# Kernel tuning notes

Measured on AMD Instinct MI355X. Metric: run time of the kernel, lower is better.

## Reference

```python
import jax, jax.numpy as jnp
import numpy as np

NEG = -1e9
BN_EPS = 1e-3  # keras BatchNormalization default epsilon
LRELU = 0.2    # GAT leaky-relu slope


def _gat(Xt, bias_mat, Wg, a1, a2, bg):
    """Dense multi-head GAT (Velickovic TF impl).
    Xt: [B,N,F], bias_mat: [B,N,N] additive mask (0 / -1e9).
    Wg: [H,F,D], a1/a2/bg: [H,D]. Returns [B,N,H*D]."""
    feats = jnp.einsum('bnf,hfd->bhnd', Xt, Wg)          # [B,H,N,D]
    f1 = jnp.einsum('bhnd,hd->bhn', feats, a1)
    f2 = jnp.einsum('bhnd,hd->bhn', feats, a2)
    logits = f1[:, :, :, None] + f2[:, :, None, :]        # [B,H,N,N]
    logits = jax.nn.leaky_relu(logits, LRELU) + bias_mat[:, None]
    coefs = jax.nn.softmax(logits, axis=-1)
    vals = jnp.einsum('bhnm,bhmd->bhnd', coefs, feats) + bg[None, :, None, :]
    vals = jax.nn.elu(vals)
    B, H, N, D = vals.shape
    return jnp.transpose(vals, (0, 2, 1, 3)).reshape(B, N, H * D)


def setup_inputs() -> dict:
    key = jax.random.key(0)
    ks = jax.random.split(key, 16)
    B, T, N, F = 4, 12, 2048, 64
    H, D = 4, 16           # attn_heads, hid_units
    C = H * D              # out_channels = 64

    X = jax.random.normal(ks[0], (B, T, N, F), dtype=jnp.float32)
    # random sparse adjacency (~avg degree 16) + self loops -> additive mask
    adj = jax.random.uniform(ks[1], (B, N, N)) < (16.0 / N)
    adj = adj | jnp.eye(N, dtype=bool)[None]
    bias_mat = jnp.where(adj, 0.0, NEG).astype(jnp.float32)

    he = lambda k, s: jax.random.normal(k, s, dtype=jnp.float32) * np.sqrt(2.0 / s[-2] if len(s) > 1 else 2.0 / s[-1])
    return {
        'X': X, 'bias_mat': bias_mat,
        'W_z': he(ks[2], (F, C)), 'Z_bias': he(ks[3], (1, C)),
        'W_h': he(ks[4], (F, C)), 'H_bias': he(ks[5], (1, C)),
        'Wg_z': he(ks[6], (H, F, D)), 'a1_z': he(ks[7], (H, D)),
        'a2_z': he(ks[8], (H, D)), 'bg_z': jnp.zeros((H, D), jnp.float32),
        'Wg_h': he(ks[9], (H, F, D)), 'a1_h': he(ks[10], (H, D)),
        'a2_h': he(ks[11], (H, D)), 'bg_h': jnp.zeros((H, D), jnp.float32),
        'bn_gamma': jnp.ones((C,), jnp.float32), 'bn_beta': jnp.zeros((C,), jnp.float32),
        'bn_mean': jnp.zeros((C,), jnp.float32), 'bn_var': jnp.ones((C,), jnp.float32),
    }


def reference(X, bias_mat, W_z, Z_bias, W_h, H_bias,
              Wg_z, a1_z, a2_z, bg_z, Wg_h, a1_h, a2_h, bg_h,
              bn_gamma, bn_beta, bn_mean, bn_var):
    B, T, N, F = X.shape
    C = W_z.shape[1]
    H0 = jnp.zeros((B, N, C), dtype=jnp.float32)

    def step(Hc, Xt):
        Z = _gat(Xt, bias_mat, Wg_z, a1_z, a2_z, bg_z) + Xt @ W_z + Z_bias + Hc
        Z = jax.nn.sigmoid(Z)
        Tt = _gat(Xt, bias_mat, Wg_h, a1_h, a2_h, bg_h) + Hc + Xt @ W_h + H_bias
        Tt = jnp.tanh(Tt)
        Hn = Z * Hc + (1.0 - Z) * Tt
        return Hn, None

    Xs = jnp.transpose(X, (1, 0, 2, 3))  # [T,B,N,F]
    Hf, _ = jax.lax.scan(step, H0, Xs)
    # last_layer=True path: BatchNorm (inference, moving stats) on final H
    out = (Hf - bn_mean) * jax.lax.rsqrt(bn_var + BN_EPS) * bn_gamma + bn_beta
    return out
```

## Files before the change

kernel.cpp:

```cpp
#include <hip/hip_runtime.h>
#include <cstdint>
#include <cstddef>

#define NB 4
#define NT 12
#define NN 2048
#define NF 64
#define NH 4
#define ND 16
#define NC 64
#define MAXD 64
#define NR (NB * NT * NN)

typedef _Float16 f16x8 __attribute__((ext_vector_type(8)));
typedef _Float16 f16x2 __attribute__((ext_vector_type(2)));
typedef float f32x4 __attribute__((ext_vector_type(4)));

#define LR(v) ((v) >= 0.f ? (v) : 0.2f * (v))
#define RCPF(x) __builtin_amdgcn_rcpf(x)

#define MACLO(acc, w, d)                                                      \
  asm("v_fma_mix_f32 %0, %1, %2, %0 op_sel:[0,0,0] op_sel_hi:[0,1,0]"         \
      : "+v"(acc) : "v"(w), "v"(d))
#define MACHI(acc, w, d)                                                      \
  asm("v_fma_mix_f32 %0, %1, %2, %0 op_sel:[0,1,0] op_sel_hi:[0,1,0]"         \
      : "+v"(acc) : "v"(w), "v"(d))

__global__ __launch_bounds__(256) void build_adj_k(const float* __restrict__ bias,
                                                   int* __restrict__ adj,
                                                   int* __restrict__ deg) {
  int gtid = blockIdx.x * 256 + threadIdx.x;
  int wid = gtid >> 6;
  int lane = threadIdx.x & 63;
  if (wid >= NB * NN) return;
  const float* row = bias + (size_t)wid * NN;
  int* arow = adj + (size_t)wid * MAXD;
  int count = 0;
  for (int c0 = 0; c0 < NN; c0 += 64) {
    float v = __builtin_nontemporal_load(row + c0 + lane);
    bool e = (v > -1e8f);
    unsigned long long m = __ballot(e);
    int pre = __popcll(m & ((1ull << lane) - 1ull));
    if (e) {
      int pos = count + pre;
      if (pos < MAXD) arow[pos] = c0 + lane;
    }
    count += __popcll(m);
  }
  if (lane == 0) deg[wid] = count < MAXD ? count : MAXD;
}

__global__ __launch_bounds__(256) void prep_w_k(
    const float* __restrict__ Wgz, const float* __restrict__ Wgh,
    const float* __restrict__ Wz,  const float* __restrict__ Wh,
    const float* __restrict__ a1z, const float* __restrict__ a2z,
    const float* __restrict__ a1h, const float* __restrict__ a2h,
    const float* __restrict__ Zb,  const float* __restrict__ Hb,
    _Float16* __restrict__ W16, float* __restrict__ biasC) {
  int idx = blockIdx.x * 256 + threadIdx.x;
  if (idx < 272 * 64) {
    int c = idx >> 6, k = idx & 63;
    float w;
    if (c < 64)       w = Wgz[((c >> 4) << 10) + (k << 4) + (c & 15)];
    else if (c < 128) { int q = c - 64; w = Wgh[((q >> 4) << 10) + (k << 4) + (q & 15)]; }
    else if (c < 192) w = Wz[(k << 6) + (c - 128)];
    else if (c < 256) w = Wh[(k << 6) + (c - 192)];
    else {
      int j = c - 256, h = j & 3;
      const float* Wg = (j & 4) ? Wgh : Wgz;
      const float* av = (j & 8) ? ((j & 4) ? a2h : a2z) : ((j & 4) ? a1h : a1z);
      float s = 0.f;
#pragma unroll
      for (int d = 0; d < 16; d++)
        s = fmaf(Wg[(h << 10) + (k << 4) + d], av[(h << 4) + d], s);
      w = s;
    }
    W16[idx] = (_Float16)w;
  }
  if (blockIdx.x == 0 && threadIdx.x < 128)
    biasC[threadIdx.x] =
        (threadIdx.x < 64) ? Zb[threadIdx.x] : Hb[threadIdx.x - 64];
}

__global__ __launch_bounds__(256) void mfma_gemm_k(
    const float* __restrict__ X, const _Float16* __restrict__ W16,
    const float* __restrict__ biasC,
    uint32_t* __restrict__ gbufF, uint32_t* __restrict__ gbufS,
    float* __restrict__ fbuf) {
  __shared__ uint32_t tr[4][16 * 68];
  const int tid = threadIdx.x;
  const int wv = tid >> 6, lane = tid & 63;
  const int m = lane & 15, quad = lane >> 4;
  const unsigned rw = blockIdx.x * 64 + wv * 16;
  uint32_t* tw = tr[wv];

  const float* xr = X + (size_t)(rw + m) * 64;
  float4 x0 = *(const float4*)(xr + quad * 8);
  float4 x1 = *(const float4*)(xr + quad * 8 + 4);
  float4 x2 = *(const float4*)(xr + 32 + quad * 8);
  float4 x3 = *(const float4*)(xr + 32 + quad * 8 + 4);
  f16x8 A0 = {(_Float16)x0.x, (_Float16)x0.y, (_Float16)x0.z, (_Float16)x0.w,
              (_Float16)x1.x, (_Float16)x1.y, (_Float16)x1.z, (_Float16)x1.w};
  f16x8 A1 = {(_Float16)x2.x, (_Float16)x2.y, (_Float16)x2.z, (_Float16)x2.w,
              (_Float16)x3.x, (_Float16)x3.y, (_Float16)x3.z, (_Float16)x3.w};

  float bzc[4], bhc[4];
#pragma unroll
  for (int j = 0; j < 4; j++) {
    bzc[j] = biasC[j * 16 + m];
    bhc[j] = biasC[64 + j * 16 + m];
  }
  const int rsub = lane >> 4, chk = lane & 15;

  f32x4 zacc[4], zs[4];
#pragma unroll
  for (int ct = 0; ct < 17; ct++) {
    const _Float16* wp = W16 + (ct * 16 + m) * 64;
    f16x8 B0 = *(const f16x8*)(wp + quad * 8);
    f16x8 B1 = *(const f16x8*)(wp + 32 + quad * 8);
    f32x4 acc = {0.f, 0.f, 0.f, 0.f};
    acc = __builtin_amdgcn_mfma_f32_16x16x32_f16(A0, B0, acc, 0, 0, 0);
    acc = __builtin_amdgcn_mfma_f32_16x16x32_f16(A1, B1, acc, 0, 0, 0);
    if (ct < 4) {
      zacc[ct] = acc;
    } else if (ct < 8) {
      const int j = ct - 4;
#pragma unroll
      for (int r = 0; r < 4; r++) {
        f16x2 pv = {(_Float16)zacc[j][r], (_Float16)acc[r]};
        tw[(quad * 4 + r) * 68 + j * 16 + m] = __builtin_bit_cast(uint32_t, pv);
      }
      if (ct == 7) {
#pragma unroll
        for (int i = 0; i < 4; i++) {
          int row = i * 4 + rsub;
          uint4 v = *(const uint4*)&tw[row * 68 + chk * 4];
          *(uint4*)&gbufF[(size_t)(rw + row) * 64 + chk * 4] = v;
        }
      }
    } else if (ct < 12) {
#pragma unroll
      for (int r = 0; r < 4; r++) zs[ct - 8][r] = acc[r] + bzc[ct - 8];
    } else if (ct < 16) {
      const int j = ct - 12;
#pragma unroll
      for (int r = 0; r < 4; r++) {
        f16x2 pv = {(_Float16)zs[j][r], (_Float16)(acc[r] + bhc[j])};
        tw[(quad * 4 + r) * 68 + j * 16 + m] = __builtin_bit_cast(uint32_t, pv);
      }
      if (ct == 15) {
#pragma unroll
        for (int i = 0; i < 4; i++) {
          int row = i * 4 + rsub;
          uint4 v = *(const uint4*)&tw[row * 68 + chk * 4];
          *(uint4*)&gbufS[(size_t)(rw + row) * 64 + chk * 4] = v;
        }
      }
    } else {
      const unsigned rb = rw + quad * 4;
#pragma unroll
      for (int r = 0; r < 4; r++) fbuf[(size_t)(rb + r) * 16 + m] = acc[r];
    }
  }
}

__global__ __launch_bounds__(256) void attn_gru_k(
    const uint32_t* __restrict__ gbufF, const uint32_t* __restrict__ gbufS,
    const float* __restrict__ fbuf,
    const int* __restrict__ adj, const int* __restrict__ deg,
    const float* __restrict__ bgz, const float* __restrict__ bgh,
    const float* __restrict__ gam, const float* __restrict__ bet,
    const float* __restrict__ mu, const float* __restrict__ var,
    float* __restrict__ out) {
  __shared__ int adjL[4][MAXD];
  __shared__ float wexp[4][8][68];
  const int tid = threadIdx.x;
  const int lane = tid & 63;
  const int ws = tid >> 6;
  const int bid = blockIdx.x;
  const int swz = (bid & 7) * (2048 / 8) + (bid >> 3);
  const int node = swz * 4 + ws;
  const int b = node >> 11;
  const int nl = node & (NN - 1);
  const int dg = deg[node];
  const int myadj = (lane < dg) ? adj[node * MAXD + lane] : 0;
  adjL[ws][lane] = myadj;
  const int dgp = (dg + 3) & ~3;
  const int ch = lane, hh = lane >> 4;
  const int sr = lane & 7, ss = lane >> 3;

#pragma unroll
  for (int k = 0; k < 8; k++) wexp[ws][k][lane] = 0.f;

  const float bz = bgz[ch], bh = bgh[ch];

  float4 c1z, c1h, c2z, c2h;
  {
    const float* fb0 = fbuf + (size_t)(b * NT) * NN * 16;
    const float4* p0 = (const float4*)(fb0 + nl * 16);
    const float4* q0 = (const float4*)(fb0 + (size_t)myadj * 16);
    c1z = p0[0]; c1h = p0[1]; c2z = q0[2]; c2h = q0[3];
  }

  float hc = 0.f;
#pragma unroll 1
  for (int t = 0; t < NT; t++) {
    const unsigned rb = (unsigned)(b * NT + t) * NN;
    const uint32_t* gF = gbufF + (size_t)rb * 64;
    const uint32_t spd = gbufS[((size_t)rb + nl) * 64 + ch];

    float e0 = __expf(LR(c1z.x + c2z.x));
    float e1 = __expf(LR(c1z.y + c2z.y));
    float e2 = __expf(LR(c1z.z + c2z.z));
    float e3 = __expf(LR(c1z.w + c2z.w));
    float e4 = __expf(LR(c1h.x + c2h.x));
    float e5 = __expf(LR(c1h.y + c2h.y));
    float e6 = __expf(LR(c1h.z + c2h.z));
    float e7 = __expf(LR(c1h.w + c2h.w));
    if (lane < dg) {
      wexp[ws][0][lane] = e0;
      wexp[ws][1][lane] = e1;
      wexp[ws][2][lane] = e2;
      wexp[ws][3][lane] = e3;
      wexp[ws][4][lane] = e4;
      wexp[ws][5][lane] = e5;
      wexp[ws][6][lane] = e6;
      wexp[ws][7][lane] = e7;
    }

    if (t + 1 < NT) {
      const float* fbn = fbuf + ((size_t)rb + NN) * 16;
      const float4* pn = (const float4*)(fbn + nl * 16);
      const float4* qn = (const float4*)(fbn + (size_t)myadj * 16);
      c1z = pn[0]; c1h = pn[1]; c2z = qn[2]; c2h = qn[3];
    }

    float4 u0 = *(const float4*)&wexp[ws][sr][ss * 8];
    float4 u1 = *(const float4*)&wexp[ws][sr][ss * 8 + 4];
    float part = ((u0.x + u0.y) + (u0.z + u0.w)) +
                 ((u1.x + u1.y) + (u1.z + u1.w));
    part += __shfl_xor(part, 8);
    part += __shfl_xor(part, 16);
    part += __shfl_xor(part, 32);
    const float rsz = RCPF(__shfl(part, hh));
    const float rsh = RCPF(__shfl(part, 4 + hh));

    float az = 0.f, ah = 0.f;
    const float* wz = wexp[ws][hh];
    const float* wh = wexp[ws][4 + hh];
    int mi = 0;
    for (; mi + 8 <= dgp; mi += 8) {
      int4 ma = *(const int4*)&adjL[ws][mi];
      int4 mb = *(const int4*)&adjL[ws][mi + 4];
      uint32_t d0 = gF[(ma.x << 6) + ch];
      uint32_t d1 = gF[(ma.y << 6) + ch];
      uint32_t d2 = gF[(ma.z << 6) + ch];
      uint32_t d3 = gF[(ma.w << 6) + ch];
      uint32_t d4 = gF[(mb.x << 6) + ch];
      uint32_t d5 = gF[(mb.y << 6) + ch];
      uint32_t d6 = gF[(mb.z << 6) + ch];
      uint32_t d7 = gF[(mb.w << 6) + ch];
      float4 wza = *(const float4*)&wz[mi];
      float4 wzb = *(const float4*)&wz[mi + 4];
      float4 wha = *(const float4*)&wh[mi];
      float4 whb = *(const float4*)&wh[mi + 4];
      MACLO(az, wza.x, d0); MACHI(ah, wha.x, d0);
      MACLO(az, wza.y, d1); MACHI(ah, wha.y, d1);
      MACLO(az, wza.z, d2); MACHI(ah, wha.z, d2);
      MACLO(az, wza.w, d3); MACHI(ah, wha.w, d3);
      MACLO(az, wzb.x, d4); MACHI(ah, whb.x, d4);
      MACLO(az, wzb.y, d5); MACHI(ah, whb.y, d5);
      MACLO(az, wzb.z, d6); MACHI(ah, whb.z, d6);
      MACLO(az, wzb.w, d7); MACHI(ah, whb.w, d7);
    }
    if (mi < dgp) {
      int4 ma = *(const int4*)&adjL[ws][mi];
      uint32_t d0 = gF[(ma.x << 6) + ch];
      uint32_t d1 = gF[(ma.y << 6) + ch];
      uint32_t d2 = gF[(ma.z << 6) + ch];
      uint32_t d3 = gF[(ma.w << 6) + ch];
      float4 wza = *(const float4*)&wz[mi];
      float4 wha = *(const float4*)&wh[mi];
      MACLO(az, wza.x, d0); MACHI(ah, wha.x, d0);
      MACLO(az, wza.y, d1); MACHI(ah, wha.y, d1);
      MACLO(az, wza.z, d2); MACHI(ah, wha.z, d2);
      MACLO(az, wza.w, d3); MACHI(ah, wha.w, d3);
    }
    az *= rsz;
    ah *= rsh;

    f16x2 sp = __builtin_bit_cast(f16x2, spd);
    float vz = az + bz; vz = vz > 0.f ? vz : __expf(vz) - 1.f;
    float vh = ah + bh; vh = vh > 0.f ? vh : __expf(vh) - 1.f;
    float zp = vz + (float)sp.x + hc;
    float tp = vh + (float)sp.y + hc;
    float zg = RCPF(1.f + __expf(-zp));
    float tg = 1.f - 2.f * RCPF(__expf(2.f * tp) + 1.f);
    hc = zg * hc + (1.f - zg) * tg;
  }

  const float bnm = mu[ch];
  const float bns = rsqrtf(var[ch] + 1e-3f);
  out[(size_t)node * 64 + ch] = (hc - bnm) * bns * gam[ch] + bet[ch];
}

extern "C" void kernel_launch(void* const* d_in, const int* in_sizes, int n_in,
                              void* d_out, int out_size, void* d_ws, size_t ws_size,
                              hipStream_t stream) {
  (void)in_sizes; (void)n_in; (void)out_size; (void)ws_size;
  const float* X   = (const float*)d_in[0];
  const float* bm  = (const float*)d_in[1];
  const float* Wz  = (const float*)d_in[2];
  const float* Zb  = (const float*)d_in[3];
  const float* Wh  = (const float*)d_in[4];
  const float* Hb  = (const float*)d_in[5];
  const float* Wgz = (const float*)d_in[6];
  const float* a1z = (const float*)d_in[7];
  const float* a2z = (const float*)d_in[8];
  const float* bgz = (const float*)d_in[9];
  const float* Wgh = (const float*)d_in[10];
  const float* a1h = (const float*)d_in[11];
  const float* a2h = (const float*)d_in[12];
  const float* bgh = (const float*)d_in[13];
  const float* gam = (const float*)d_in[14];
  const float* bet = (const float*)d_in[15];
  const float* mu  = (const float*)d_in[16];
  const float* var = (const float*)d_in[17];
  float* out = (float*)d_out;

  char* p = (char*)d_ws;
  uint32_t* gbufF = (uint32_t*)p; p += (size_t)NR * 64 * sizeof(uint32_t);
  uint32_t* gbufS = (uint32_t*)p; p += (size_t)NR * 64 * sizeof(uint32_t);
  float*    fbuf  = (float*)p;    p += (size_t)NR * 16 * sizeof(float);
  int*      adj   = (int*)p;      p += (size_t)NB * NN * MAXD * sizeof(int);
  int*      deg   = (int*)p;      p += (size_t)NB * NN * sizeof(int);
  _Float16* W16   = (_Float16*)p; p += 272 * 64 * sizeof(_Float16);
  float*    biasC = (float*)p;    p += 128 * sizeof(float);

  prep_w_k<<<dim3(68), dim3(256), 0, stream>>>(
      Wgz, Wgh, Wz, Wh, a1z, a2z, a1h, a2h, Zb, Hb, W16, biasC);
  build_adj_k<<<dim3(NB * NN / 4), dim3(256), 0, stream>>>(bm, adj, deg);
  mfma_gemm_k<<<dim3(NR / 64), dim3(256), 0, stream>>>(
      X, W16, biasC, gbufF, gbufS, fbuf);
  attn_gru_k<<<dim3(NB * NN / 4), dim3(256), 0, stream>>>(
      gbufF, gbufS, fbuf, adj, deg, bgz, bgh, gam, bet, mu, var, out);
}
```

Baseline: 238.0 us.

## Use persistent waves with atomic work stealing and hoisted neighbor gather offsets

After: 437.0 us. 1.84x slower.

```diff
diff --git a/kernel.cpp b/kernel.cpp
--- a/kernel.cpp
+++ b/kernel.cpp
@@ -28,7 +28,9 @@
 
 __global__ __launch_bounds__(256) void build_adj_k(const float* __restrict__ bias,
                                                    int* __restrict__ adj,
-                                                   int* __restrict__ deg) {
+                                                   int* __restrict__ deg,
+                                                   int* __restrict__ ctr) {
+  if (blockIdx.x < 8 && threadIdx.x == 0) ctr[blockIdx.x] = 0;
   int gtid = blockIdx.x * 256 + threadIdx.x;
   int wid = gtid >> 6;
   int lane = threadIdx.x & 63;
@@ -164,144 +166,254 @@
   }
 }
 
-__global__ __launch_bounds__(256) void attn_gru_k(
+__global__ __launch_bounds__(256, 4) void attn_gru_k(
     const uint32_t* __restrict__ gbufF, const uint32_t* __restrict__ gbufS,
     const float* __restrict__ fbuf,
     const int* __restrict__ adj, const int* __restrict__ deg,
     const float* __restrict__ bgz, const float* __restrict__ bgh,
     const float* __restrict__ gam, const float* __restrict__ bet,
     const float* __restrict__ mu, const float* __restrict__ var,
-    float* __restrict__ out) {
+    int* __restrict__ ctr, float* __restrict__ out) {
   __shared__ int adjL[4][MAXD];
   __shared__ float wexp[4][8][68];
   const int tid = threadIdx.x;
   const int lane = tid & 63;
   const int ws = tid >> 6;
-  const int bid = blockIdx.x;
-  const int swz = (bid & 7) * (2048 / 8) + (bid >> 3);
-  const int node = swz * 4 + ws;
-  const int b = node >> 11;
-  const int nl = node & (NN - 1);
-  const int dg = deg[node];
-  const int myadj = (lane < dg) ? adj[node * MAXD + lane] : 0;
-  adjL[ws][lane] = myadj;
-  const int dgp = (dg + 3) & ~3;
+  const int g = blockIdx.x & 7;
   const int ch = lane, hh = lane >> 4;
+  const uint32_t ch4 = (uint32_t)ch << 2;
   const int sr = lane & 7, ss = lane >> 3;
 
-#pragma unroll
-  for (int k = 0; k < 8; k++) wexp[ws][k][lane] = 0.f;
-
   const float bz = bgz[ch], bh = bgh[ch];
-
-  float4 c1z, c1h, c2z, c2h;
-  {
-    const float* fb0 = fbuf + (size_t)(b * NT) * NN * 16;
-    const float4* p0 = (const float4*)(fb0 + nl * 16);
-    const float4* q0 = (const float4*)(fb0 + (size_t)myadj * 16);
-    c1z = p0[0]; c1h = p0[1]; c2z = q0[2]; c2h = q0[3];
-  }
-
-  float hc = 0.f;
-#pragma unroll 1
-  for (int t = 0; t < NT; t++) {
-    const unsigned rb = (unsigned)(b * NT + t) * NN;
-    const uint32_t* gF = gbufF + (size_t)rb * 64;
-    const uint32_t spd = gbufS[((size_t)rb + nl) * 64 + ch];
-
-    float e0 = __expf(LR(c1z.x + c2z.x));
-    float e1 = __expf(LR(c1z.y + c2z.y));
-    float e2 = __expf(LR(c1z.z + c2z.z));
-    float e3 = __expf(LR(c1z.w + c2z.w));
-    float e4 = __expf(LR(c1h.x + c2h.x));
-    float e5 = __expf(LR(c1h.y + c2h.y));
-    float e6 = __expf(LR(c1h.z + c2h.z));
-    float e7 = __expf(LR(c1h.w + c2h.w));
-    if (lane < dg) {
-      wexp[ws][0][lane] = e0;
-      wexp[ws][1][lane] = e1;
-      wexp[ws][2][lane] = e2;
-      wexp[ws][3][lane] = e3;
-      wexp[ws][4][lane] = e4;
-      wexp[ws][5][lane] = e5;
-      wexp[ws][6][lane] = e6;
-      wexp[ws][7][lane] = e7;
-    }
-
-    if (t + 1 < NT) {
-      const float* fbn = fbuf + ((size_t)rb + NN) * 16;
-      const float4* pn = (const float4*)(fbn + nl * 16);
-      const float4* qn = (const float4*)(fbn + (size_t)myadj * 16);
-      c1z = pn[0]; c1h = pn[1]; c2z = qn[2]; c2h = qn[3];
-    }
-
-    float4 u0 = *(const float4*)&wexp[ws][sr][ss * 8];
-    float4 u1 = *(const float4*)&wexp[ws][sr][ss * 8 + 4];
-    float part = ((u0.x + u0.y) + (u0.z + u0.w)) +
-                 ((u1.x + u1.y) + (u1.z + u1.w));
-    part += __shfl_xor(part, 8);
-    part += __shfl_xor(part, 16);
-    part += __shfl_xor(part, 32);
-    const float rsz = RCPF(__shfl(part, hh));
-    const float rsh = RCPF(__shfl(part, 4 + hh));
-
-    float az = 0.f, ah = 0.f;
-    const float* wz = wexp[ws][hh];
-    const float* wh = wexp[ws][4 + hh];
-    int mi = 0;
-    for (; mi + 8 <= dgp; mi += 8) {
-      int4 ma = *(const int4*)&adjL[ws][mi];
-      int4 mb = *(const int4*)&adjL[ws][mi + 4];
-      uint32_t d0 = gF[(ma.x << 6) + ch];
-      uint32_t d1 = gF[(ma.y << 6) + ch];
-      uint32_t d2 = gF[(ma.z << 6) + ch];
-      uint32_t d3 = gF[(ma.w << 6) + ch];
-      uint32_t d4 = gF[(mb.x << 6) + ch];
-      uint32_t d5 = gF[(mb.y << 6) + ch];
-      uint32_t d6 = gF[(mb.z << 6) + ch];
-      uint32_t d7 = gF[(mb.w << 6) + ch];
-      float4 wza = *(const float4*)&wz[mi];
-      float4 wzb = *(const float4*)&wz[mi + 4];
-      float4 wha = *(const float4*)&wh[mi];
-      float4 whb = *(const float4*)&wh[mi + 4];
-      MACLO(az, wza.x, d0); MACHI(ah, wha.x, d0);
-      MACLO(az, wza.y, d1); MACHI(ah, wha.y, d1);
-      MACLO(az, wza.z, d2); MACHI(ah, wha.z, d2);
-      MACLO(az, wza.w, d3); MACHI(ah, wha.w, d3);
-      MACLO(az, wzb.x, d4); MACHI(ah, whb.x, d4);
-      MACLO(az, wzb.y, d5); MACHI(ah, whb.y, d5);
-      MACLO(az, wzb.z, d6); MACHI(ah, whb.z, d6);
-      MACLO(az, wzb.w, d7); MACHI(ah, whb.w, d7);
-    }
-    if (mi < dgp) {
-      int4 ma = *(const int4*)&adjL[ws][mi];
-      uint32_t d0 = gF[(ma.x << 6) + ch];
-      uint32_t d1 = gF[(ma.y << 6) + ch];
-      uint32_t d2 = gF[(ma.z << 6) + ch];
-      uint32_t d3 = gF[(ma.w << 6) + ch];
-      float4 wza = *(const float4*)&wz[mi];
-      float4 wha = *(const float4*)&wh[mi];
-      MACLO(az, wza.x, d0); MACHI(ah, wha.x, d0);
-      MACLO(az, wza.y, d1); MACHI(ah, wha.y, d1);
-      MACLO(az, wza.z, d2); MACHI(ah, wha.z, d2);
-      MACLO(az, wza.w, d3); MACHI(ah, wha.w, d3);
-    }
-    az *= rsz;
-    ah *= rsh;
-
-    f16x2 sp = __builtin_bit_cast(f16x2, spd);
-    float vz = az + bz; vz = vz > 0.f ? vz : __expf(vz) - 1.f;
-    float vh = ah + bh; vh = vh > 0.f ? vh : __expf(vh) - 1.f;
-    float zp = vz + (float)sp.x + hc;
-    float tp = vh + (float)sp.y + hc;
-    float zg = RCPF(1.f + __expf(-zp));
-    float tg = 1.f - 2.f * RCPF(__expf(2.f * tp) + 1.f);
-    hc = zg * hc + (1.f - zg) * tg;
-  }
-
   const float bnm = mu[ch];
   const float bns = rsqrtf(var[ch] + 1e-3f);
-  out[(size_t)node * 64 + ch] = (hc - bnm) * bns * gam[ch] + bet[ch];
+  const float bng = gam[ch], bnb = bet[ch];
+
+  int* ctrg = ctr + g;
+  for (;;) {
+    int tk = 0;
+    if (lane == 0) tk = atomicAdd(ctrg, 1);
+    tk = __shfl(tk, 0);
+    if (tk >= NN * NB / 8) break;
+    const int node = g * (NN * NB / 8) + tk;
+    const int b = node >> 11;
+    const int nl = node & (NN - 1);
+    const int dg = deg[node];
+    const int myadj = (lane < dg) ? adj[node * MAXD + lane] : 0;
+    adjL[ws][lane] = myadj;
+    const int dgp4 = (dg + 3) & ~3;
+    const int dgp8 = (dg + 7) & ~7;
+
+#pragma unroll
+    for (int k = 0; k < 8; k++) wexp[ws][k][lane] = 0.f;
+
+    uint4 o0, o1, o2, o3, o4, o5, o6, o7;
+    {
+      int4 A0 = *(const int4*)&adjL[ws][0];
+      int4 A1 = *(const int4*)&adjL[ws][4];
+      o0 = {(uint32_t)(A0.x << 8) + ch4, (uint32_t)(A0.y << 8) + ch4,
+            (uint32_t)(A0.z << 8) + ch4, (uint32_t)(A0.w << 8) + ch4};
+      o1 = {(uint32_t)(A1.x << 8) + ch4, (uint32_t)(A1.y << 8) + ch4,
+            (uint32_t)(A1.z << 8) + ch4, (uint32_t)(A1.w << 8) + ch4};
+      if (dgp8 > 8) {
+        int4 A2 = *(const int4*)&adjL[ws][8];
+        int4 A3 = *(const int4*)&adjL[ws][12];
+        o2 = {(uint32_t)(A2.x << 8) + ch4, (uint32_t)(A2.y << 8) + ch4,
+              (uint32_t)(A2.z << 8) + ch4, (uint32_t)(A2.w << 8) + ch4};
+        o3 = {(uint32_t)(A3.x << 8) + ch4, (uint32_t)(A3.y << 8) + ch4,
+              (uint32_t)(A3.z << 8) + ch4, (uint32_t)(A3.w << 8) + ch4};
+      }
+      if (dgp8 > 16) {
+        int4 A4 = *(const int4*)&adjL[ws][16];
+        int4 A5 = *(const int4*)&adjL[ws][20];
+        o4 = {(uint32_t)(A4.x << 8) + ch4, (uint32_t)(A4.y << 8) + ch4,
+              (uint32_t)(A4.z << 8) + ch4, (uint32_t)(A4.w << 8) + ch4};
+        o5 = {(uint32_t)(A5.x << 8) + ch4, (uint32_t)(A5.y << 8) + ch4,
+              (uint32_t)(A5.z << 8) + ch4, (uint32_t)(A5.w << 8) + ch4};
+      }
+      if (dgp8 > 24) {
+        int4 A6 = *(const int4*)&adjL[ws][24];
+        int4 A7 = *(const int4*)&adjL[ws][28];
+        o6 = {(uint32_t)(A6.x << 8) + ch4, (uint32_t)(A6.y << 8) + ch4,
+              (uint32_t)(A6.z << 8) + ch4, (uint32_t)(A6.w << 8) + ch4};
+        o7 = {(uint32_t)(A7.x << 8) + ch4, (uint32_t)(A7.y << 8) + ch4,
+              (uint32_t)(A7.z << 8) + ch4, (uint32_t)(A7.w << 8) + ch4};
+      }
+    }
+
+    float4 c1z, c1h, c2z, c2h;
+    {
+      const float* fb0 = fbuf + (size_t)(b * NT) * NN * 16;
+      const float4* p0 = (const float4*)(fb0 + nl * 16);
+      const float4* q0 = (const float4*)(fb0 + (size_t)myadj * 16);
+      c1z = p0[0]; c1h = p0[1]; c2z = q0[2]; c2h = q0[3];
+    }
+
+    float hc = 0.f;
+#pragma unroll 1
+    for (int t = 0; t < NT; t++) {
+      const unsigned rb = (unsigned)(b * NT + t) * NN;
+      const uint32_t* gF = gbufF + (size_t)rb * 64;
+      const uint32_t spd = gbufS[((size_t)rb + nl) * 64 + ch];
+
+      float e0 = __expf(LR(c1z.x + c2z.x));
+      float e1 = __expf(LR(c1z.y + c2z.y));
+      float e2 = __expf(LR(c1z.z + c2z.z));
+      float e3 = __expf(LR(c1z.w + c2z.w));
+      float e4 = __expf(LR(c1h.x + c2h.x));
+      float e5 = __expf(LR(c1h.y + c2h.y));
+      float e6 = __expf(LR(c1h.z + c2h.z));
+      float e7 = __expf(LR(c1h.w + c2h.w));
+      if (lane < dg) {
+        wexp[ws][0][lane] = e0;
+        wexp[ws][1][lane] = e1;
+        wexp[ws][2][lane] = e2;
+        wexp[ws][3][lane] = e3;
+        wexp[ws][4][lane] = e4;
+        wexp[ws][5][lane] = e5;
+        wexp[ws][6][lane] = e6;
+        wexp[ws][7][lane] = e7;
+      }
+
+      if (t + 1 < NT) {
+        const float* fbn = fbuf + ((size_t)rb + NN) * 16;
+        const float4* pn = (const float4*)(fbn + nl * 16);
+        const float4* qn = (const float4*)(fbn + (size_t)myadj * 16);
+        c1z = pn[0]; c1h = pn[1]; c2z = qn[2]; c2h = qn[3];
+      }
+
+      float4 u0 = *(const float4*)&wexp[ws][sr][ss * 8];
+      float4 u1 = *(const float4*)&wexp[ws][sr][ss * 8 + 4];
+      float part = ((u0.x + u0.y) + (u0.z + u0.w)) +
+                   ((u1.x + u1.y) + (u1.z + u1.w));
+      part += __shfl_xor(part, 8);
+      part += __shfl_xor(part, 16);
+      part += __shfl_xor(part, 32);
+      const float rsz = RCPF(__shfl(part, hh));
+      const float rsh = RCPF(__shfl(part, 4 + hh));
+
+      float az = 0.f, ah = 0.f;
+      const float* wz = wexp[ws][hh];
+      const float* wh = wexp[ws][4 + hh];
+      const char* gFb = (const char*)gF;
+      uint32_t d00, d01, d02, d03, d04, d05, d06, d07;
+      uint32_t d10, d11, d12, d13, d14, d15, d16, d17;
+      uint32_t d20, d21, d22, d23, d24, d25, d26, d27;
+      uint32_t d30, d31, d32, d33, d34, d35, d36, d37;
+      d00 = *(const uint32_t*)(gFb + o0.x);
+      d01 = *(const uint32_t*)(gFb + o0.y);
+      d02 = *(const uint32_t*)(gFb + o0.z);
+      d03 = *(const uint32_t*)(gFb + o0.w);
+      d04 = *(const uint32_t*)(gFb + o1.x);
+      d05 = *(const uint32_t*)(gFb + o1.y);
+      d06 = *(const uint32_t*)(gFb + o1.z);
+      d07 = *(const uint32_t*)(gFb + o1.w);
+      if (dgp8 > 8) {
+        d10 = *(const uint32_t*)(gFb + o2.x);
+        d11 = *(const uint32_t*)(gFb + o2.y);
+        d12 = *(const uint32_t*)(gFb + o2.z);
+        d13 = *(const uint32_t*)(gFb + o2.w);
+        d14 = *(const uint32_t*)(gFb + o3.x);
+        d15 = *(const uint32_t*)(gFb + o3.y);
+        d16 = *(const uint32_t*)(gFb + o3.z);
+        d17 = *(const uint32_t*)(gFb + o3.w);
+      }
+      if (dgp8 > 16) {
+        d20 = *(const uint32_t*)(gFb + o4.x);
+        d21 = *(const uint32_t*)(gFb + o4.y);
+        d22 = *(const uint32_t*)(gFb + o4.z);
+        d23 = *(const uint32_t*)(gFb + o4.w);
+        d24 = *(const uint32_t*)(gFb + o5.x);
+        d25 = *(const uint32_t*)(gFb + o5.y);
+        d26 = *(const uint32_t*)(gFb + o5.z);
+        d27 = *(const uint32_t*)(gFb + o5.w);
+      }
+      if (dgp8 > 24) {
+        d30 = *(const uint32_t*)(gFb + o6.x);
+        d31 = *(const uint32_t*)(gFb + o6.y);
+        d32 = *(const uint32_t*)(gFb + o6.z);
+        d33 = *(const uint32_t*)(gFb + o6.w);
+        d34 = *(const uint32_t*)(gFb + o7.x);
+        d35 = *(const uint32_t*)(gFb + o7.y);
+        d36 = *(const uint32_t*)(gFb + o7.z);
+        d37 = *(const uint32_t*)(gFb + o7.w);
+      }
+      {
+        float4 wza = *(const float4*)&wz[0], wzb = *(const float4*)&wz[4];
+        float4 wha = *(const float4*)&wh[0], whb = *(const float4*)&wh[4];
+        MACLO(az, wza.x, d00); MACHI(ah, wha.x, d00);
+        MACLO(az, wza.y, d01); MACHI(ah, wha.y, d01);
+        MACLO(az, wza.z, d02); MACHI(ah, wha.z, d02);
+        MACLO(az, wza.w, d03); MACHI(ah, wha.w, d03);
+        MACLO(az, wzb.x, d04); MACHI(ah, whb.x, d04);
+        MACLO(az, wzb.y, d05); MACHI(ah, whb.y, d05);
+        MACLO(az, wzb.z, d06); MACHI(ah, whb.z, d06);
+        MACLO(az, wzb.w, d07); MACHI(ah, whb.w, d07);
+      }
+      if (dgp8 > 8) {
+        float4 wza = *(const float4*)&wz[8], wzb = *(const float4*)&wz[12];
+        float4 wha = *(const float4*)&wh[8], whb = *(const float4*)&wh[12];
+        MACLO(az, wza.x, d10); MACHI(ah, wha.x, d10);
+        MACLO(az, wza.y, d11); MACHI(ah, wha.y, d11);
+        MACLO(az, wza.z, d12); MACHI(ah, wha.z, d12);
+        MACLO(az, wza.w, d13); MACHI(ah, wha.w, d13);
+        MACLO(az, wzb.x, d14); MACHI(ah, whb.x, d14);
+        MACLO(az, wzb.y, d15); MACHI(ah, whb.y, d15);
+        MACLO(az, wzb.z, d16); MACHI(ah, whb.z, d16);
+        MACLO(az, wzb.w, d17); MACHI(ah, whb.w, d17);
+      }
+      if (dgp8 > 16) {
+        float4 wza = *(const float4*)&wz[16], wzb = *(const float4*)&wz[20];
+        float4 wha = *(const float4*)&wh[16], whb = *(const float4*)&wh[20];
+        MACLO(az, wza.x, d20); MACHI(ah, wha.x, d20);
+        MACLO(az, wza.y, d21); MACHI(ah, wha.y, d21);
+        MACLO(az, wza.z, d22); MACHI(ah, wha.z, d22);
+        MACLO(az, wza.w, d23); MACHI(ah, wha.w, d23);
+        MACLO(az, wzb.x, d24); MACHI(ah, whb.x, d24);
+        MACLO(az, wzb.y, d25); MACHI(ah, whb.y, d25);
+        MACLO(az, wzb.z, d26); MACHI(ah, whb.z, d26);
+        MACLO(az, wzb.w, d27); MACHI(ah, whb.w, d27);
+      }
+      if (dgp8 > 24) {
+        float4 wza = *(const float4*)&wz[24], wzb = *(const float4*)&wz[28];
+        float4 wha = *(const float4*)&wh[24], whb = *(const float4*)&wh[28];
+        MACLO(az, wza.x, d30); MACHI(ah, wha.x, d30);
+        MACLO(az, wza.y, d31); MACHI(ah, wha.y, d31);
+        MACLO(az, wza.z, d32); MACHI(ah, wha.z, d32);
+        MACLO(az, wza.w, d33); MACHI(ah, wha.w, d33);
+        MACLO(az, wzb.x, d34); MACHI(ah, whb.x, d34);
+        MACLO(az, wzb.y, d35); MACHI(ah, whb.y, d35);
+        MACLO(az, wzb.z, d36); MACHI(ah, whb.z, d36);
+        MACLO(az, wzb.w, d37); MACHI(ah, whb.w, d37);
+      }
+      for (int mi = 32; mi < dgp4; mi += 4) {
+        int4 ma = *(const int4*)&adjL[ws][mi];
+        uint32_t t0 = gF[(ma.x << 6) + ch];
+        uint32_t t1 = gF[(ma.y << 6) + ch];
+        uint32_t t2 = gF[(ma.z << 6) + ch];
+        uint32_t t3 = gF[(ma.w << 6) + ch];
+        float4 wza = *(const float4*)&wz[mi];
+        float4 wha = *(const float4*)&wh[mi];
+        MACLO(az, wza.x, t0); MACHI(ah, wha.x, t0);
+        MACLO(az, wza.y, t1); MACHI(ah, wha.y, t1);
+        MACLO(az, wza.z, t2); MACHI(ah, wha.z, t2);
+        MACLO(az, wza.w, t3); MACHI(ah, wha.w, t3);
+      }
+      az *= rsz;
+      ah *= rsh;
+
+      f16x2 sp = __builtin_bit_cast(f16x2, spd);
+      float vz = az + bz; vz = vz > 0.f ? vz : __expf(vz) - 1.f;
+      float vh = ah + bh; vh = vh > 0.f ? vh : __expf(vh) - 1.f;
+      float zp = vz + (float)sp.x + hc;
+      float tp = vh + (float)sp.y + hc;
+      float zg = RCPF(1.f + __expf(-zp));
+      float tg = 1.f - 2.f * RCPF(__expf(2.f * tp) + 1.f);
+      hc = zg * hc + (1.f - zg) * tg;
+    }
+
+    out[(size_t)node * 64 + ch] = (hc - bnm) * bns * bng + bnb;
+  }
 }
 
 extern "C" void kernel_launch(void* const* d_in, const int* in_sizes, int n_in,
@@ -336,12 +448,13 @@
   int*      deg   = (int*)p;      p += (size_t)NB * NN * sizeof(int);
   _Float16* W16   = (_Float16*)p; p += 272 * 64 * sizeof(_Float16);
   float*    biasC = (float*)p;    p += 128 * sizeof(float);
+  int*      ctr   = (int*)p;      p += 8 * sizeof(int);
 
   prep_w_k<<<dim3(68), dim3(256), 0, stream>>>(
       Wgz, Wgh, Wz, Wh, a1z, a2z, a1h, a2h, Zb, Hb, W16, biasC);
-  build_adj_k<<<dim3(NB * NN / 4), dim3(256), 0, stream>>>(bm, adj, deg);
+  build_adj_k<<<dim3(NB * NN / 4), dim3(256), 0, stream>>>(bm, adj, deg, ctr);
   mfma_gemm_k<<<dim3(NR / 64), dim3(256), 0, stream>>>(
       X, W16, biasC, gbufF, gbufS, fbuf);
-  attn_gru_k<<<dim3(NB * NN / 4), dim3(256), 0, stream>>>(
-      gbufF, gbufS, fbuf, adj, deg, bgz, bgh, gam, bet, mu, var, out);
+  attn_gru_k<<<dim3(1024), dim3(256), 0, stream>>>(
+      gbufF, gbufS, fbuf, adj, deg, bgz, bgh, gam, bet, mu, var, ctr, out);
 }
```
